# Performance work log

Measured on AMD Instinct MI355X. Metric: run time of the kernel, lower is better.

## Reference

```python
import jax, jax.numpy as jnp
import numpy as np

D_EMB, D_PROJ, N_HEADS, HIDDEN = 640, 256, 4, 128
HEAD_DIM = D_PROJ // N_HEADS
B = 65536
EPS = 1e-5


def setup_inputs() -> dict:
    key = jax.random.key(0)
    ks = jax.random.split(key, 14)
    def w(k, shape, fan_in):
        return (jax.random.normal(k, shape, jnp.float32) / np.sqrt(fan_in)).astype(jnp.float32)
    return {
        "global_diff": jax.random.normal(ks[0], (B, D_EMB), jnp.float32),
        "local_diff": jax.random.normal(ks[1], (B, D_EMB), jnp.float32),
        # global/local projections ([in, out] layout; math identical to torch Linear)
        "Wg": w(ks[2], (D_EMB, D_PROJ), D_EMB), "bg": jnp.zeros((D_PROJ,), jnp.float32),
        "Wl": w(ks[3], (D_EMB, D_PROJ), D_EMB), "bl": jnp.zeros((D_PROJ,), jnp.float32),
        # MultiheadAttention packed in-proj (q|k|v) and out-proj
        "W_in": w(ks[4], (D_PROJ, 3 * D_PROJ), D_PROJ), "b_in": jnp.zeros((3 * D_PROJ,), jnp.float32),
        "W_out": w(ks[5], (D_PROJ, D_PROJ), D_PROJ), "b_out": jnp.zeros((D_PROJ,), jnp.float32),
        # LayerNorm
        "gamma": jnp.ones((D_PROJ,), jnp.float32), "beta": jnp.zeros((D_PROJ,), jnp.float32),
        # MLP head
        "W1": w(ks[6], (D_PROJ, HIDDEN), D_PROJ), "b1": jnp.zeros((HIDDEN,), jnp.float32),
        "W2": w(ks[7], (HIDDEN, 1), HIDDEN), "b2": jnp.zeros((1,), jnp.float32),
    }


def reference(global_diff, local_diff, Wg, bg, Wl, bl, W_in, b_in, W_out, b_out,
              gamma, beta, W1, b1, W2, b2):
    # projections (eval mode: dropout inactive)
    g = global_diff @ Wg + bg              # [B, P] -- the single query token
    l = local_diff @ Wl + bl               # [B, P]
    kv = jnp.stack([g, l], axis=1)         # [B, 2, P]

    Wq, Wk, Wv = jnp.split(W_in, 3, axis=1)
    bq, bk, bv = jnp.split(b_in, 3)
    b = g.shape[0]
    q = (g @ Wq + bq).reshape(b, N_HEADS, HEAD_DIM)        # [B, H, d]
    k = (kv @ Wk + bk).reshape(b, 2, N_HEADS, HEAD_DIM)    # [B, 2, H, d]
    v = (kv @ Wv + bv).reshape(b, 2, N_HEADS, HEAD_DIM)

    scale = 1.0 / np.sqrt(HEAD_DIM)
    scores = jnp.einsum('bhd,bshd->bhs', q, k) * scale     # [B, H, 2]
    attn = jax.nn.softmax(scores, axis=-1)
    ctx = jnp.einsum('bhs,bshd->bhd', attn, v).reshape(b, D_PROJ)
    attended = ctx @ W_out + b_out                         # [B, P]

    # residual + LayerNorm (eps=1e-5, torch default)
    x = g + attended
    mu = jnp.mean(x, axis=-1, keepdims=True)
    var = jnp.mean(jnp.square(x - mu), axis=-1, keepdims=True)
    y = (x - mu) * jax.lax.rsqrt(var + EPS) * gamma + beta

    # MLP head: Linear -> exact GELU (torch default) -> Linear
    h = jax.nn.gelu(y @ W1 + b1, approximate=False)
    out = (h @ W2 + b2).squeeze(-1)                        # [B]
    return out
```

## Files before the change

### kernel.cpp

```cpp
#include <hip/hip_runtime.h>
#include <math.h>

typedef __attribute__((ext_vector_type(4))) float f32x4;
typedef __attribute__((ext_vector_type(8))) __bf16 bf16x8;

static constexpr int WG_OFF = 0;
static constexpr int WL_OFF = 163840;
static constexpr int WQ_OFF = 327680;
static constexpr int WK_OFF = 393216;
static constexpr int WV_OFF = 458752;
static constexpr int WO_OFF = 524288;
static constexpr int W1_OFF = 589824;
static constexpr int W_TOTAL = 622592;

__device__ __forceinline__ unsigned short f2bf(float f) {
  unsigned u = __builtin_bit_cast(unsigned, f);
  u += 0x7FFFu + ((u >> 16) & 1u);
  return (unsigned short)(u >> 16);
}

__device__ __forceinline__ f32x4 mfma16(bf16x8 a, bf16x8 b, f32x4 c) {
  return __builtin_amdgcn_mfma_f32_16x16x32_bf16(a, b, c, 0, 0, 0);
}
__device__ __forceinline__ f32x4 fzero4() {
  f32x4 v; v[0] = 0.f; v[1] = 0.f; v[2] = 0.f; v[3] = 0.f; return v;
}

__device__ __forceinline__ bf16x8 ldB(const unsigned short* __restrict__ ws, int fragIdx, int lane) {
  return *(const bf16x8*)(ws + (size_t)(fragIdx * 64 + lane) * 8);
}

template <int STRIDE>
__device__ __forceinline__ bf16x8 ldA(const char* s, int row, int kbyte) {
  return *(const bf16x8*)(s + row * STRIDE + (kbyte ^ ((row & 7) << 4)));
}

__device__ __forceinline__ void stC(char* s, int row, int col, float v) {
  *(__bf16*)(s + row * 512 + ((col * 2) ^ ((row & 7) << 4))) = (__bf16)v;
}
__device__ __forceinline__ float ldC(const char* s, int row, int col) {
  return (float)*(const __bf16*)(s + row * 512 + ((col * 2) ^ ((row & 7) << 4)));
}

__device__ __forceinline__ bf16x8 cvt8(float4 a, float4 b) {
  bf16x8 t;
  t[0] = (__bf16)a.x; t[1] = (__bf16)a.y; t[2] = (__bf16)a.z; t[3] = (__bf16)a.w;
  t[4] = (__bf16)b.x; t[5] = (__bf16)b.y; t[6] = (__bf16)b.z; t[7] = (__bf16)b.w;
  return t;
}

template <int N>
__device__ __forceinline__ void red16(float* v) {
#pragma unroll
  for (int m = 1; m < 16; m <<= 1) {
#pragma unroll
    for (int i = 0; i < N; ++i) v[i] += __shfl_xor(v[i], m);
  }
}

__device__ __forceinline__ void stageA32(const float* __restrict__ A, char* sA, int tid) {
#pragma unroll
  for (int i = 0; i < 5; ++i) {
    const int idx = i * 512 + tid;
    const int row = idx / 80;
    const int c8 = idx - row * 80;
    const float* ap = A + (size_t)idx * 8;
    float4 f0 = *(const float4*)ap;
    float4 f1 = *(const float4*)(ap + 4);
    *(bf16x8*)(sA + row * 1280 + ((c8 * 16) ^ ((row & 7) << 4))) = cvt8(f0, f1);
  }
}

__device__ __forceinline__ void proj640(const char* sA, const unsigned short* __restrict__ wsW,
                                        const float* __restrict__ bias, char* sDst,
                                        int f0, int lane) {
  const int l15 = lane & 15, kg4 = lane >> 4;
  f32x4 acc[2][2];
#pragma unroll
  for (int m = 0; m < 2; ++m)
#pragma unroll
    for (int n = 0; n < 2; ++n) acc[m][n] = fzero4();
#pragma unroll 2
  for (int kt = 0; kt < 20; ++kt) {
    bf16x8 b0 = ldB(wsW, kt * 16 + f0, lane);
    bf16x8 b1 = ldB(wsW, kt * 16 + f0 + 1, lane);
    const int kb = kt * 64 + kg4 * 16;
#pragma unroll
    for (int m = 0; m < 2; ++m) {
      bf16x8 a = ldA<1280>(sA, m * 16 + l15, kb);
      acc[m][0] = mfma16(a, b0, acc[m][0]);
      acc[m][1] = mfma16(a, b1, acc[m][1]);
    }
  }
#pragma unroll
  for (int n = 0; n < 2; ++n) {
    const int col = (f0 + n) * 16 + l15;
    const float bv = bias[col];
#pragma unroll
    for (int m = 0; m < 2; ++m)
#pragma unroll
      for (int r = 0; r < 4; ++r)
        stC(sDst, m * 16 + kg4 * 4 + r, col, acc[m][n][r] + bv);
  }
}

__device__ __forceinline__ void gemm256(const char* sA, const unsigned short* __restrict__ wsW,
                                        int f0, f32x4 (&acc)[2][2], int lane) {
  const int l15 = lane & 15, kg4 = lane >> 4;
#pragma unroll 2
  for (int kt = 0; kt < 8; ++kt) {
    bf16x8 b0 = ldB(wsW, kt * 16 + f0, lane);
    bf16x8 b1 = ldB(wsW, kt * 16 + f0 + 1, lane);
    const int kb = kt * 64 + kg4 * 16;
#pragma unroll
    for (int m = 0; m < 2; ++m) {
      bf16x8 a = ldA<512>(sA, m * 16 + l15, kb);
      acc[m][0] = mfma16(a, b0, acc[m][0]);
      acc[m][1] = mfma16(a, b1, acc[m][1]);
    }
  }
}

__global__ void convert_w(const float* __restrict__ Wg, const float* __restrict__ Wl,
                          const float* __restrict__ Win, const float* __restrict__ Wout,
                          const float* __restrict__ W1, unsigned short* __restrict__ ws) {
  const int tid = blockIdx.x * 256 + threadIdx.x;
  if (tid >= W_TOTAL) return;
  const float* src;
  int stride, coloff, base, lognf;
  if (tid < WL_OFF)      { src = Wg;   stride = 256; coloff = 0;   base = WG_OFF; lognf = 4; }
  else if (tid < WQ_OFF) { src = Wl;   stride = 256; coloff = 0;   base = WL_OFF; lognf = 4; }
  else if (tid < WK_OFF) { src = Win;  stride = 768; coloff = 0;   base = WQ_OFF; lognf = 4; }
  else if (tid < WV_OFF) { src = Win;  stride = 768; coloff = 256; base = WK_OFF; lognf = 4; }
  else if (tid < WO_OFF) { src = Win;  stride = 768; coloff = 512; base = WV_OFF; lognf = 4; }
  else if (tid < W1_OFF) { src = Wout; stride = 256; coloff = 0;   base = WO_OFF; lognf = 4; }
  else                   { src = W1;   stride = 128; coloff = 0;   base = W1_OFF; lognf = 3; }
  const int idx = tid - base;
  const int j = idx & 7;
  const int lane = (idx >> 3) & 63;
  const int fl = idx >> 9;
  const int n = fl & ((1 << lognf) - 1);
  const int kt = fl >> lognf;
  const int k = kt * 32 + (lane >> 4) * 8 + j;
  const int col = coloff + n * 16 + (lane & 15);
  ws[tid] = f2bf(src[k * stride + col]);
}

__global__ __launch_bounds__(512)
__attribute__((amdgpu_waves_per_eu(4, 4)))
void dca_fused(
    const float* __restrict__ gdiff, const float* __restrict__ ldiff,
    const float* __restrict__ bg, const float* __restrict__ bl,
    const float* __restrict__ bin, const float* __restrict__ bout,
    const float* __restrict__ gamma, const float* __restrict__ beta,
    const float* __restrict__ b1, const float* __restrict__ W2,
    const float* __restrict__ b2, const unsigned short* __restrict__ wsw,
    float* __restrict__ out) {
  __shared__ __align__(16) char sMem[73728];
  char* sA = sMem;
  char* sG = sMem + 40960;
  char* sL = sMem + 57344;
  float* sSc = (float*)sMem;
  float* sLN = (float*)(sMem + 2048);
  float* sMu = (float*)(sMem + 4096);
  float* sPO = (float*)(sMem + 4352);
  char* sQ = sMem + 8192;

  const int tid = threadIdx.x;
  const int blk = blockIdx.x;
  const int lane = tid & 63, l15 = lane & 15, kg4 = lane >> 4;
  const int w = tid >> 6;
  const int f0 = w * 2;

  stageA32(gdiff + (size_t)blk * 32 * 640, sA, tid);
  __syncthreads();
  proj640(sA, wsw + WG_OFF, bg, sG, f0, lane);
  __syncthreads();
  stageA32(ldiff + (size_t)blk * 32 * 640, sA, tid);
  __syncthreads();
  proj640(sA, wsw + WL_OFF, bl, sL, f0, lane);
  __syncthreads();

  {
    f32x4 qa[2][2];
#pragma unroll
    for (int m = 0; m < 2; ++m) { qa[m][0] = fzero4(); qa[m][1] = fzero4(); }
    gemm256(sG, wsw + WQ_OFF, f0, qa, lane);
#pragma unroll
    for (int m = 0; m < 2; ++m) {
      bf16x8 t;
#pragma unroll
      for (int n = 0; n < 2; ++n) {
        const float bv = bin[(f0 + n) * 16 + l15];
#pragma unroll
        for (int r = 0; r < 4; ++r) t[n * 4 + r] = (__bf16)(qa[m][n][r] + bv);
      }
      *(bf16x8*)(sQ + m * 8192 + tid * 16) = t;
    }
  }

  float s[16];
  {
    f32x4 kk[2][2];
#pragma unroll
    for (int m = 0; m < 2; ++m) { kk[m][0] = fzero4(); kk[m][1] = fzero4(); }
    gemm256(sG, wsw + WK_OFF, f0, kk, lane);
#pragma unroll
    for (int m = 0; m < 2; ++m) {
      bf16x8 t = *(const bf16x8*)(sQ + m * 8192 + tid * 16);
#pragma unroll
      for (int r = 0; r < 4; ++r)
        s[m * 4 + r] = (float)t[r] * kk[m][0][r] + (float)t[4 + r] * kk[m][1][r];
    }
#pragma unroll
    for (int m = 0; m < 2; ++m) { kk[m][0] = fzero4(); kk[m][1] = fzero4(); }
    gemm256(sL, wsw + WK_OFF, f0, kk, lane);
#pragma unroll
    for (int m = 0; m < 2; ++m) {
      bf16x8 t = *(const bf16x8*)(sQ + m * 8192 + tid * 16);
#pragma unroll
      for (int r = 0; r < 4; ++r)
        s[8 + m * 4 + r] = (float)t[r] * kk[m][0][r] + (float)t[4 + r] * kk[m][1][r];
    }
  }
  red16<16>(s);
  if (l15 < 2) {
#pragma unroll
    for (int r = 0; r < 4; ++r) {
      const int row = l15 * 16 + kg4 * 4 + r;
      sSc[(w * 32 + row) * 2 + 0] = s[l15 * 4 + r];
      sSc[(w * 32 + row) * 2 + 1] = s[8 + l15 * 4 + r];
    }
  }
  __syncthreads();
  float a0[2][4], a1[2][4];
  {
    const int pw = w ^ 1;
#pragma unroll
    for (int m = 0; m < 2; ++m)
#pragma unroll
      for (int r = 0; r < 4; ++r) {
        const int row = m * 16 + kg4 * 4 + r;
        const float t0 = s[m * 4 + r] + sSc[(pw * 32 + row) * 2 + 0];
        const float t1 = s[8 + m * 4 + r] + sSc[(pw * 32 + row) * 2 + 1];
        const float d = (t0 - t1) * 0.125f;
        const float t = 1.0f / (1.0f + expf(d));
        a1[m][r] = t;
        a0[m][r] = 1.0f - t;
      }
  }

  f32x4 ctx[2][2];
  {
    f32x4 vv[2][2];
#pragma unroll
    for (int m = 0; m < 2; ++m) { vv[m][0] = fzero4(); vv[m][1] = fzero4(); }
    gemm256(sG, wsw + WV_OFF, f0, vv, lane);
#pragma unroll
    for (int n = 0; n < 2; ++n)
#pragma unroll
      for (int m = 0; m < 2; ++m)
#pragma unroll
        for (int r = 0; r < 4; ++r) ctx[m][n][r] = a0[m][r] * vv[m][n][r];
#pragma unroll
    for (int m = 0; m < 2; ++m) { vv[m][0] = fzero4(); vv[m][1] = fzero4(); }
    gemm256(sL, wsw + WV_OFF, f0, vv, lane);
#pragma unroll
    for (int n = 0; n < 2; ++n) {
      const float bv = bin[512 + (f0 + n) * 16 + l15];
#pragma unroll
      for (int m = 0; m < 2; ++m)
#pragma unroll
        for (int r = 0; r < 4; ++r) ctx[m][n][r] += a1[m][r] * vv[m][n][r] + bv;
    }
  }
  __syncthreads();
#pragma unroll
  for (int n = 0; n < 2; ++n) {
    const int col = (f0 + n) * 16 + l15;
#pragma unroll
    for (int m = 0; m < 2; ++m)
#pragma unroll
      for (int r = 0; r < 4; ++r)
        stC(sL, m * 16 + kg4 * 4 + r, col, ctx[m][n][r]);
  }
  __syncthreads();

  {
    f32x4 at[2][2];
#pragma unroll
    for (int m = 0; m < 2; ++m) { at[m][0] = fzero4(); at[m][1] = fzero4(); }
    gemm256(sL, wsw + WO_OFF, f0, at, lane);
    float st[16];
#pragma unroll
    for (int i = 0; i < 16; ++i) st[i] = 0.f;
#pragma unroll
    for (int n = 0; n < 2; ++n) {
      const int col = (f0 + n) * 16 + l15;
      const float bv = bout[col];
#pragma unroll
      for (int m = 0; m < 2; ++m)
#pragma unroll
        for (int r = 0; r < 4; ++r) {
          const int row = m * 16 + kg4 * 4 + r;
          const float x = at[m][n][r] + bv + ldC(sG, row, col);
          stC(sG, row, col, x);
          st[m * 4 + r] += x;
          st[8 + m * 4 + r] += x * x;
        }
    }
    red16<16>(st);
    if (l15 < 2) {
#pragma unroll
      for (int r = 0; r < 4; ++r) {
        const int row = l15 * 16 + kg4 * 4 + r;
        sLN[(w * 32 + row) * 2 + 0] = st[l15 * 4 + r];
        sLN[(w * 32 + row) * 2 + 1] = st[8 + l15 * 4 + r];
      }
    }
  }
  __syncthreads();
  if (tid < 64) {
    const int row = tid >> 1, j = tid & 1;
    float v = 0.f;
#pragma unroll
    for (int ww = 0; ww < 8; ++ww) v += sLN[(ww * 32 + row) * 2 + j];
    sMu[row * 2 + j] = v;
  }
  __syncthreads();
#pragma unroll
  for (int n = 0; n < 2; ++n) {
    const int col = (f0 + n) * 16 + l15;
    const float ga = gamma[col], be = beta[col];
#pragma unroll
    for (int m = 0; m < 2; ++m)
#pragma unroll
      for (int r = 0; r < 4; ++r) {
        const int row = m * 16 + kg4 * 4 + r;
        const float m_ = sMu[row * 2 + 0] * (1.0f / 256.0f);
        const float var = sMu[row * 2 + 1] * (1.0f / 256.0f) - m_ * m_;
        const float x = ldC(sG, row, col);
        stC(sG, row, col, (x - m_) * rsqrtf(var + 1e-5f) * ga + be);
      }
  }
  __syncthreads();

  f32x4 ha[2];
  ha[0] = fzero4();
  ha[1] = fzero4();
#pragma unroll 2
  for (int kt = 0; kt < 8; ++kt) {
    bf16x8 b = ldB(wsw + W1_OFF, kt * 8 + w, lane);
    const int kb = kt * 64 + kg4 * 16;
#pragma unroll
    for (int m = 0; m < 2; ++m) {
      bf16x8 a = ldA<512>(sG, m * 16 + l15, kb);
      ha[m] = mfma16(a, b, ha[m]);
    }
  }
  {
    const int colh = w * 16 + l15;
    const float bv1 = b1[colh], w2v = W2[colh];
    float o[8];
#pragma unroll
    for (int m = 0; m < 2; ++m)
#pragma unroll
      for (int r = 0; r < 4; ++r) {
        float hv = ha[m][r] + bv1;
        hv = 0.5f * hv * (1.0f + erff(hv * 0.70710678118654752f));
        o[m * 4 + r] = hv * w2v;
      }
    red16<8>(o);
    if (l15 < 2) {
#pragma unroll
      for (int r = 0; r < 4; ++r)
        sPO[w * 32 + l15 * 16 + kg4 * 4 + r] = o[l15 * 4 + r];
    }
  }
  __syncthreads();
  if (tid < 32) {
    float acc = b2[0];
#pragma unroll
    for (int ww = 0; ww < 8; ++ww) acc += sPO[ww * 32 + tid];
    out[(size_t)blk * 32 + tid] = acc;
  }
}

extern "C" void kernel_launch(void* const* d_in, const int* in_sizes, int n_in,
                              void* d_out, int out_size, void* d_ws, size_t ws_size,
                              hipStream_t stream) {
  (void)in_sizes; (void)n_in; (void)out_size; (void)ws_size;
  const float* gdiff = (const float*)d_in[0];
  const float* ldiff = (const float*)d_in[1];
  const float* Wg    = (const float*)d_in[2];
  const float* bg    = (const float*)d_in[3];
  const float* Wl    = (const float*)d_in[4];
  const float* bl    = (const float*)d_in[5];
  const float* Win   = (const float*)d_in[6];
  const float* bin   = (const float*)d_in[7];
  const float* Wout  = (const float*)d_in[8];
  const float* bout  = (const float*)d_in[9];
  const float* gamma = (const float*)d_in[10];
  const float* beta  = (const float*)d_in[11];
  const float* W1    = (const float*)d_in[12];
  const float* b1    = (const float*)d_in[13];
  const float* W2    = (const float*)d_in[14];
  const float* b2    = (const float*)d_in[15];
  unsigned short* ws = (unsigned short*)d_ws;
  float* out = (float*)d_out;

  convert_w<<<dim3((W_TOTAL + 255) / 256), dim3(256), 0, stream>>>(Wg, Wl, Win, Wout, W1, ws);
  dca_fused<<<dim3(2048), dim3(512), 0, stream>>>(gdiff, ldiff, bg, bl, bin, bout, gamma,
                                                  beta, b1, W2, b2,
                                                  (const unsigned short*)ws, out);
}
```

Measured before the change: 214.3 us.

## Split K staging in halves and keep Q in registers to raise occupancy

Input tiles are staged and projected in two 320-column halves, halving the LDS staging buffer. The Q projection result stays in registers instead of a shared buffer, and the per-wave partial scores are written to shared memory and reread after the barrier. Total LDS drops so more workgroups fit per CU, and the waves-per-EU hint is raised to match. In exchange there are extra barriers per projection and higher register pressure from holding Q across the K GEMMs.

```diff
diff --git a/kernel.cpp b/kernel.cpp
--- a/kernel.cpp
+++ b/kernel.cpp
@@ -58,40 +58,37 @@
   }
 }
 
-__device__ __forceinline__ void stageA32(const float* __restrict__ A, char* sA, int tid) {
-#pragma unroll
-  for (int i = 0; i < 5; ++i) {
-    const int idx = i * 512 + tid;
-    const int row = idx / 80;
-    const int c8 = idx - row * 80;
-    const float* ap = A + (size_t)idx * 8;
+__device__ __forceinline__ void stageHalf(const float* __restrict__ A, int half, char* sA, int tid) {
+  for (int c = tid; c < 1280; c += 512) {
+    const int row = c / 40;
+    const int c8 = c - row * 40;
+    const float* ap = A + (size_t)row * 640 + half * 320 + c8 * 8;
     float4 f0 = *(const float4*)ap;
     float4 f1 = *(const float4*)(ap + 4);
-    *(bf16x8*)(sA + row * 1280 + ((c8 * 16) ^ ((row & 7) << 4))) = cvt8(f0, f1);
-  }
-}
-
-__device__ __forceinline__ void proj640(const char* sA, const unsigned short* __restrict__ wsW,
-                                        const float* __restrict__ bias, char* sDst,
-                                        int f0, int lane) {
+    *(bf16x8*)(sA + row * 640 + ((c8 * 16) ^ ((row & 7) << 4))) = cvt8(f0, f1);
+  }
+}
+
+__device__ __forceinline__ void projHalf(const char* sA, const unsigned short* __restrict__ wsW,
+                                         int ktBase, f32x4 (&acc)[2][2], int f0, int lane) {
   const int l15 = lane & 15, kg4 = lane >> 4;
-  f32x4 acc[2][2];
-#pragma unroll
-  for (int m = 0; m < 2; ++m)
-#pragma unroll
-    for (int n = 0; n < 2; ++n) acc[m][n] = fzero4();
 #pragma unroll 2
-  for (int kt = 0; kt < 20; ++kt) {
-    bf16x8 b0 = ldB(wsW, kt * 16 + f0, lane);
-    bf16x8 b1 = ldB(wsW, kt * 16 + f0 + 1, lane);
+  for (int kt = 0; kt < 10; ++kt) {
+    bf16x8 b0 = ldB(wsW, (ktBase + kt) * 16 + f0, lane);
+    bf16x8 b1 = ldB(wsW, (ktBase + kt) * 16 + f0 + 1, lane);
     const int kb = kt * 64 + kg4 * 16;
 #pragma unroll
     for (int m = 0; m < 2; ++m) {
-      bf16x8 a = ldA<1280>(sA, m * 16 + l15, kb);
+      bf16x8 a = ldA<640>(sA, m * 16 + l15, kb);
       acc[m][0] = mfma16(a, b0, acc[m][0]);
       acc[m][1] = mfma16(a, b1, acc[m][1]);
     }
   }
+}
+
+__device__ __forceinline__ void writeTile(f32x4 (&acc)[2][2], const float* __restrict__ bias,
+                                          char* sDst, int f0, int lane) {
+  const int l15 = lane & 15, kg4 = lane >> 4;
 #pragma unroll
   for (int n = 0; n < 2; ++n) {
     const int col = (f0 + n) * 16 + l15;
@@ -147,7 +144,7 @@
 }
 
 __global__ __launch_bounds__(512)
-__attribute__((amdgpu_waves_per_eu(4, 4)))
+__attribute__((amdgpu_waves_per_eu(6)))
 void dca_fused(
     const float* __restrict__ gdiff, const float* __restrict__ ldiff,
     const float* __restrict__ bg, const float* __restrict__ bl,
@@ -156,15 +153,14 @@
     const float* __restrict__ b1, const float* __restrict__ W2,
     const float* __restrict__ b2, const unsigned short* __restrict__ wsw,
     float* __restrict__ out) {
-  __shared__ __align__(16) char sMem[73728];
+  __shared__ __align__(16) char sMem[53248];
   char* sA = sMem;
-  char* sG = sMem + 40960;
-  char* sL = sMem + 57344;
+  char* sG = sMem + 20480;
+  char* sL = sMem + 36864;
   float* sSc = (float*)sMem;
   float* sLN = (float*)(sMem + 2048);
   float* sMu = (float*)(sMem + 4096);
   float* sPO = (float*)(sMem + 4352);
-  char* sQ = sMem + 8192;
 
   const int tid = threadIdx.x;
   const int blk = blockIdx.x;
@@ -172,68 +168,85 @@
   const int w = tid >> 6;
   const int f0 = w * 2;
 
-  stageA32(gdiff + (size_t)blk * 32 * 640, sA, tid);
-  __syncthreads();
-  proj640(sA, wsw + WG_OFF, bg, sG, f0, lane);
-  __syncthreads();
-  stageA32(ldiff + (size_t)blk * 32 * 640, sA, tid);
-  __syncthreads();
-  proj640(sA, wsw + WL_OFF, bl, sL, f0, lane);
-  __syncthreads();
-
-  {
-    f32x4 qa[2][2];
-#pragma unroll
-    for (int m = 0; m < 2; ++m) { qa[m][0] = fzero4(); qa[m][1] = fzero4(); }
-    gemm256(sG, wsw + WQ_OFF, f0, qa, lane);
-#pragma unroll
-    for (int m = 0; m < 2; ++m) {
-      bf16x8 t;
-#pragma unroll
-      for (int n = 0; n < 2; ++n) {
-        const float bv = bin[(f0 + n) * 16 + l15];
-#pragma unroll
-        for (int r = 0; r < 4; ++r) t[n * 4 + r] = (__bf16)(qa[m][n][r] + bv);
-      }
-      *(bf16x8*)(sQ + m * 8192 + tid * 16) = t;
-    }
-  }
-
-  float s[16];
+  const float* Ag = gdiff + (size_t)blk * 32 * 640;
+  const float* Al = ldiff + (size_t)blk * 32 * 640;
+
+  {
+    f32x4 acc[2][2];
+#pragma unroll
+    for (int m = 0; m < 2; ++m) { acc[m][0] = fzero4(); acc[m][1] = fzero4(); }
+    stageHalf(Ag, 0, sA, tid);
+    __syncthreads();
+    projHalf(sA, wsw + WG_OFF, 0, acc, f0, lane);
+    __syncthreads();
+    stageHalf(Ag, 1, sA, tid);
+    __syncthreads();
+    projHalf(sA, wsw + WG_OFF, 10, acc, f0, lane);
+    writeTile(acc, bg, sG, f0, lane);
+    __syncthreads();
+#pragma unroll
+    for (int m = 0; m < 2; ++m) { acc[m][0] = fzero4(); acc[m][1] = fzero4(); }
+    stageHalf(Al, 0, sA, tid);
+    __syncthreads();
+    projHalf(sA, wsw + WL_OFF, 0, acc, f0, lane);
+    __syncthreads();
+    stageHalf(Al, 1, sA, tid);
+    __syncthreads();
+    projHalf(sA, wsw + WL_OFF, 10, acc, f0, lane);
+    writeTile(acc, bl, sL, f0, lane);
+    __syncthreads();
+  }
+
+  f32x4 q[2][2];
+#pragma unroll
+  for (int m = 0; m < 2; ++m) { q[m][0] = fzero4(); q[m][1] = fzero4(); }
+  gemm256(sG, wsw + WQ_OFF, f0, q, lane);
+#pragma unroll
+  for (int n = 0; n < 2; ++n) {
+    const float bv = bin[(f0 + n) * 16 + l15];
+#pragma unroll
+    for (int m = 0; m < 2; ++m)
+#pragma unroll
+      for (int r = 0; r < 4; ++r) q[m][n][r] += bv;
+  }
   {
     f32x4 kk[2][2];
 #pragma unroll
     for (int m = 0; m < 2; ++m) { kk[m][0] = fzero4(); kk[m][1] = fzero4(); }
     gemm256(sG, wsw + WK_OFF, f0, kk, lane);
-#pragma unroll
-    for (int m = 0; m < 2; ++m) {
-      bf16x8 t = *(const bf16x8*)(sQ + m * 8192 + tid * 16);
+    float sg[8];
+#pragma unroll
+    for (int m = 0; m < 2; ++m)
 #pragma unroll
       for (int r = 0; r < 4; ++r)
-        s[m * 4 + r] = (float)t[r] * kk[m][0][r] + (float)t[4 + r] * kk[m][1][r];
+        sg[m * 4 + r] = q[m][0][r] * kk[m][0][r] + q[m][1][r] * kk[m][1][r];
+    red16<8>(sg);
+    if (l15 == 0) {
+#pragma unroll
+      for (int m = 0; m < 2; ++m)
+#pragma unroll
+        for (int r = 0; r < 4; ++r)
+          sSc[(w * 32 + m * 16 + kg4 * 4 + r) * 2 + 0] = sg[m * 4 + r];
     }
 #pragma unroll
     for (int m = 0; m < 2; ++m) { kk[m][0] = fzero4(); kk[m][1] = fzero4(); }
     gemm256(sL, wsw + WK_OFF, f0, kk, lane);
 #pragma unroll
-    for (int m = 0; m < 2; ++m) {
-      bf16x8 t = *(const bf16x8*)(sQ + m * 8192 + tid * 16);
+    for (int m = 0; m < 2; ++m)
 #pragma unroll
       for (int r = 0; r < 4; ++r)
-        s[8 + m * 4 + r] = (float)t[r] * kk[m][0][r] + (float)t[4 + r] * kk[m][1][r];
-    }
-  }
-  red16<16>(s);
-  if (l15 < 2) {
-#pragma unroll
-    for (int r = 0; r < 4; ++r) {
-      const int row = l15 * 16 + kg4 * 4 + r;
-      sSc[(w * 32 + row) * 2 + 0] = s[l15 * 4 + r];
-      sSc[(w * 32 + row) * 2 + 1] = s[8 + l15 * 4 + r];
-    }
-  }
-  __syncthreads();
-  float a0[2][4], a1[2][4];
+        sg[m * 4 + r] = q[m][0][r] * kk[m][0][r] + q[m][1][r] * kk[m][1][r];
+    red16<8>(sg);
+    if (l15 == 0) {
+#pragma unroll
+      for (int m = 0; m < 2; ++m)
+#pragma unroll
+        for (int r = 0; r < 4; ++r)
+          sSc[(w * 32 + m * 16 + kg4 * 4 + r) * 2 + 1] = sg[m * 4 + r];
+    }
+  }
+  __syncthreads();
+  float a1v[2][4];
   {
     const int pw = w ^ 1;
 #pragma unroll
@@ -241,15 +254,11 @@
 #pragma unroll
       for (int r = 0; r < 4; ++r) {
         const int row = m * 16 + kg4 * 4 + r;
-        const float t0 = s[m * 4 + r] + sSc[(pw * 32 + row) * 2 + 0];
-        const float t1 = s[8 + m * 4 + r] + sSc[(pw * 32 + row) * 2 + 1];
-        const float d = (t0 - t1) * 0.125f;
-        const float t = 1.0f / (1.0f + expf(d));
-        a1[m][r] = t;
-        a0[m][r] = 1.0f - t;
+        const float t0 = sSc[(w * 32 + row) * 2 + 0] + sSc[(pw * 32 + row) * 2 + 0];
+        const float t1 = sSc[(w * 32 + row) * 2 + 1] + sSc[(pw * 32 + row) * 2 + 1];
+        a1v[m][r] = 1.0f / (1.0f + expf((t0 - t1) * 0.125f));
       }
   }
-
   f32x4 ctx[2][2];
   {
     f32x4 vv[2][2];
@@ -261,7 +270,7 @@
 #pragma unroll
       for (int m = 0; m < 2; ++m)
 #pragma unroll
-        for (int r = 0; r < 4; ++r) ctx[m][n][r] = a0[m][r] * vv[m][n][r];
+        for (int r = 0; r < 4; ++r) ctx[m][n][r] = (1.0f - a1v[m][r]) * vv[m][n][r];
 #pragma unroll
     for (int m = 0; m < 2; ++m) { vv[m][0] = fzero4(); vv[m][1] = fzero4(); }
     gemm256(sL, wsw + WV_OFF, f0, vv, lane);
@@ -271,7 +280,7 @@
 #pragma unroll
       for (int m = 0; m < 2; ++m)
 #pragma unroll
-        for (int r = 0; r < 4; ++r) ctx[m][n][r] += a1[m][r] * vv[m][n][r] + bv;
+        for (int r = 0; r < 4; ++r) ctx[m][n][r] += a1v[m][r] * vv[m][n][r] + bv;
     }
   }
   __syncthreads();
```

Result: slower. 241.1 us (+12.5%).
